# Performance work log

Measured on AMD Instinct MI355X. Metric: run time of the kernel, lower is better.

The kernel has to match this reference:

```python
import jax, jax.numpy as jnp
import numpy as np

B, C, H, W = 8, 512, 64, 64
M = C // 8  # query/key channels
EPS = 1e-6

def setup_inputs() -> dict:
    key = jax.random.key(0)
    ks = jax.random.split(key, 8)
    s_in = 0.02
    return {
        "x": jax.random.normal(ks[0], (B, C, H, W), dtype=jnp.float32),
        "Wq": jax.random.normal(ks[1], (M, C), dtype=jnp.float32) * s_in,
        "bq": jnp.zeros((M,), dtype=jnp.float32),
        "Wk": jax.random.normal(ks[2], (M, C), dtype=jnp.float32) * s_in,
        "bk": jnp.zeros((M,), dtype=jnp.float32),
        "Wv": jax.random.normal(ks[3], (C, C), dtype=jnp.float32) * s_in,
        "bv": jnp.zeros((C,), dtype=jnp.float32),
        "gamma": jax.random.uniform(ks[4], (1,), dtype=jnp.float32) * 0.5,
    }

def _l2_norm(t):
    # normalize over channel dim (axis=-2), per position; matches torch.norm(p=2, dim=-2)
    return t / jnp.linalg.norm(t, axis=-2, keepdims=True)

def reference(x, Wq, bq, Wk, bk, Wv, bv, gamma):
    b, c, h, w = x.shape
    n = h * w
    xf = x.reshape(b, c, n)                               # [b,c,n]
    # 1x1 convs as channel GEMMs
    Q = jnp.einsum('mc,bcn->bmn', Wq, xf) + bq[None, :, None]   # [b,m,n]
    K = jnp.einsum('mc,bcn->bmn', Wk, xf) + bk[None, :, None]   # [b,m,n]
    V = jnp.einsum('dc,bcn->bdn', Wv, xf) + bv[None, :, None]   # [b,c,n]
    Qn = _l2_norm(Q).transpose(0, 2, 1)                   # [b,n,m]
    Kn = _l2_norm(K)                                      # [b,m,n]
    # denominator: 1 / (N + Q . sum_n(K))
    tailor = 1.0 / (n + jnp.einsum('bnm,bm->bn', Qn, Kn.sum(axis=-1) + EPS))  # [b,n]
    value_sum = V.sum(axis=-1)                            # [b,c]
    matrix = jnp.einsum('bmn,bcn->bmc', Kn, V)            # [b,m,c] (O(N) contraction)
    matrix_sum = value_sum[:, :, None] + jnp.einsum('bnm,bmc->bcn', Qn, matrix)  # [b,c,n]
    weight_value = matrix_sum * tailor[:, None, :]        # [b,c,n]
    return x + gamma * weight_value.reshape(b, c, h, w)
```

## Files before the change

### kernel.cpp

```cpp
#include <hip/hip_runtime.h>
#include <hip/hip_bf16.h>

constexpr int B = 8;
constexpr int C = 512;
constexpr int M = 64;
constexpr int N = 4096;
constexpr float EPS = 1e-6f;
constexpr int NTS = 16;
constexpr int LDP = 72;
constexpr int LDPF = 68;

typedef __attribute__((ext_vector_type(8))) short short8v;
typedef __attribute__((ext_vector_type(4))) short short4v;
typedef __attribute__((ext_vector_type(4))) float f32x4;

__device__ __forceinline__ short f2b(float f) {
  union { __hip_bfloat16 h; short s; } u;
  u.h = __float2bfloat16(f);
  return u.s;
}
__device__ __forceinline__ float b2f(short s) {
  union { __hip_bfloat16 h; short s2; } u;
  u.s2 = s;
  return __bfloat162float(u.h);
}

__global__ __launch_bounds__(256) void prep_kernel(
    const float* __restrict__ Wq, const float* __restrict__ Wk,
    const float* __restrict__ Wv, short* __restrict__ Wq_bf,
    short* __restrict__ Wk_bf, short* __restrict__ Wv_bf,
    float* __restrict__ Ksum, float* __restrict__ xsum) {
  const int id = blockIdx.x * 256 + threadIdx.x;
  const int stride = gridDim.x * 256;
  for (int i = id; i < C * M / 4; i += stride) {
    const float4 a = reinterpret_cast<const float4*>(Wq)[i];
    const float4 b = reinterpret_cast<const float4*>(Wk)[i];
    short4v sa = {f2b(a.x), f2b(a.y), f2b(a.z), f2b(a.w)};
    short4v sb = {f2b(b.x), f2b(b.y), f2b(b.z), f2b(b.w)};
    reinterpret_cast<short4v*>(Wq_bf)[i] = sa;
    reinterpret_cast<short4v*>(Wk_bf)[i] = sb;
  }
  for (int i = id; i < C * C / 4; i += stride) {
    const float4 a = reinterpret_cast<const float4*>(Wv)[i];
    short4v sa = {f2b(a.x), f2b(a.y), f2b(a.z), f2b(a.w)};
    reinterpret_cast<short4v*>(Wv_bf)[i] = sa;
  }
  for (int i = id; i < B * M + B * C; i += stride) {
    if (i < B * M) Ksum[i] = 0.f;
    else xsum[i - B * M] = 0.f;
  }
}

__global__ __launch_bounds__(256) void qk_kernel(
    const float* __restrict__ x, const short* __restrict__ Wq_bf,
    const float* __restrict__ bq, const short* __restrict__ Wk_bf,
    const float* __restrict__ bk, short* __restrict__ QnT,
    short* __restrict__ KnB, float* __restrict__ Ksum) {
  __shared__ short aq[64 * LDP];
  __shared__ short ak[64 * LDP];
  __shared__ short bx[64 * LDP];
  __shared__ float colred[2][4][64];
  __shared__ float rsq[2][64];
  const int t = threadIdx.x;
  const int n0 = blockIdx.x * 64;
  const int b = blockIdx.y;
  const int w = t >> 6, l = t & 63, l15 = l & 15, kg = l >> 4;
  const int sr = t >> 2, sko = (t & 3) * 16;
  const int cr = t & 63, ng = t >> 6;
  f32x4 accQ[4], accK[4];
#pragma unroll
  for (int i = 0; i < 4; ++i) { accQ[i] = f32x4{0.f, 0.f, 0.f, 0.f}; accK[i] = f32x4{0.f, 0.f, 0.f, 0.f}; }

  short8v wq0, wq1, wk0, wk1;
  float4 xr[4];
  {
    wq0 = *reinterpret_cast<const short8v*>(&Wq_bf[sr * C + sko]);
    wq1 = *reinterpret_cast<const short8v*>(&Wq_bf[sr * C + sko + 8]);
    wk0 = *reinterpret_cast<const short8v*>(&Wk_bf[sr * C + sko]);
    wk1 = *reinterpret_cast<const short8v*>(&Wk_bf[sr * C + sko + 8]);
    const float* xg = x + ((size_t)b * C + cr) * N + n0 + ng * 16;
#pragma unroll
    for (int i = 0; i < 4; ++i) xr[i] = *reinterpret_cast<const float4*>(xg + 4 * i);
  }
  for (int c0 = 0; c0 < C; c0 += 64) {
    __syncthreads();
    *reinterpret_cast<short8v*>(&aq[sr * LDP + sko]) = wq0;
    *reinterpret_cast<short8v*>(&aq[sr * LDP + sko + 8]) = wq1;
    *reinterpret_cast<short8v*>(&ak[sr * LDP + sko]) = wk0;
    *reinterpret_cast<short8v*>(&ak[sr * LDP + sko + 8]) = wk1;
#pragma unroll
    for (int i = 0; i < 4; ++i) {
      bx[(ng * 16 + 4 * i + 0) * LDP + cr] = f2b(xr[i].x);
      bx[(ng * 16 + 4 * i + 1) * LDP + cr] = f2b(xr[i].y);
      bx[(ng * 16 + 4 * i + 2) * LDP + cr] = f2b(xr[i].z);
      bx[(ng * 16 + 4 * i + 3) * LDP + cr] = f2b(xr[i].w);
    }
    __syncthreads();
    if (c0 + 64 < C) {
      const int c1 = c0 + 64;
      wq0 = *reinterpret_cast<const short8v*>(&Wq_bf[sr * C + c1 + sko]);
      wq1 = *reinterpret_cast<const short8v*>(&Wq_bf[sr * C + c1 + sko + 8]);
      wk0 = *reinterpret_cast<const short8v*>(&Wk_bf[sr * C + c1 + sko]);
      wk1 = *reinterpret_cast<const short8v*>(&Wk_bf[sr * C + c1 + sko + 8]);
      const float* xg = x + ((size_t)b * C + c1 + cr) * N + n0 + ng * 16;
#pragma unroll
      for (int i = 0; i < 4; ++i) xr[i] = *reinterpret_cast<const float4*>(xg + 4 * i);
    }
#pragma unroll
    for (int ks = 0; ks < 2; ++ks) {
      const short8v afq = *reinterpret_cast<const short8v*>(&aq[(w * 16 + l15) * LDP + ks * 32 + kg * 8]);
      const short8v afk = *reinterpret_cast<const short8v*>(&ak[(w * 16 + l15) * LDP + ks * 32 + kg * 8]);
#pragma unroll
      for (int tc = 0; tc < 4; ++tc) {
        const short8v bf = *reinterpret_cast<const short8v*>(&bx[(tc * 16 + l15) * LDP + ks * 32 + kg * 8]);
        accQ[tc] = __builtin_amdgcn_mfma_f32_16x16x32_bf16(afq, bf, accQ[tc], 0, 0, 0);
        accK[tc] = __builtin_amdgcn_mfma_f32_16x16x32_bf16(afk, bf, accK[tc], 0, 0, 0);
      }
    }
  }
  {
    const float4 q4 = *reinterpret_cast<const float4*>(&bq[w * 16 + kg * 4]);
    const float4 k4 = *reinterpret_cast<const float4*>(&bk[w * 16 + kg * 4]);
    const float bqa[4] = {q4.x, q4.y, q4.z, q4.w};
    const float bka[4] = {k4.x, k4.y, k4.z, k4.w};
#pragma unroll
    for (int tc = 0; tc < 4; ++tc)
#pragma unroll
      for (int r = 0; r < 4; ++r) { accQ[tc][r] += bqa[r]; accK[tc][r] += bka[r]; }
  }
#pragma unroll
  for (int tc = 0; tc < 4; ++tc) {
    float vq = accQ[tc][0] * accQ[tc][0] + accQ[tc][1] * accQ[tc][1] +
               accQ[tc][2] * accQ[tc][2] + accQ[tc][3] * accQ[tc][3];
    float vk = accK[tc][0] * accK[tc][0] + accK[tc][1] * accK[tc][1] +
               accK[tc][2] * accK[tc][2] + accK[tc][3] * accK[tc][3];
    vq += __shfl_xor(vq, 16, 64); vq += __shfl_xor(vq, 32, 64);
    vk += __shfl_xor(vk, 16, 64); vk += __shfl_xor(vk, 32, 64);
    if (l < 16) { colred[0][w][tc * 16 + l] = vq; colred[1][w][tc * 16 + l] = vk; }
  }
  __syncthreads();
  if (t < 128) {
    const int which = t >> 6, n = t & 63;
    const float s = colred[which][0][n] + colred[which][1][n] +
                    colred[which][2][n] + colred[which][3][n];
    rsq[which][n] = 1.0f / sqrtf(s);
  }
  __syncthreads();
  float ksr[4] = {0.f, 0.f, 0.f, 0.f};
#pragma unroll
  for (int tc = 0; tc < 4; ++tc) {
    const float rq = rsq[0][tc * 16 + l15], rk = rsq[1][tc * 16 + l15];
#pragma unroll
    for (int r = 0; r < 4; ++r) { accQ[tc][r] *= rq; accK[tc][r] *= rk; ksr[r] += accK[tc][r]; }
  }
#pragma unroll
  for (int r = 0; r < 4; ++r) {
    float s = ksr[r];
    s += __shfl_xor(s, 1, 64); s += __shfl_xor(s, 2, 64);
    s += __shfl_xor(s, 4, 64); s += __shfl_xor(s, 8, 64);
    if (l15 == 0) atomicAdd(&Ksum[b * M + w * 16 + kg * 4 + r], s);
  }
#pragma unroll
  for (int tc = 0; tc < 4; ++tc) {
    short4v q4 = {f2b(accQ[tc][0]), f2b(accQ[tc][1]), f2b(accQ[tc][2]), f2b(accQ[tc][3])};
    *reinterpret_cast<short4v*>(&aq[(tc * 16 + l15) * LDP + w * 16 + kg * 4]) = q4;
#pragma unroll
    for (int r = 0; r < 4; ++r)
      ak[(w * 16 + kg * 4 + r) * LDP + tc * 16 + l15] = f2b(accK[tc][r]);
  }
  __syncthreads();
  {
    short* qg = QnT + ((size_t)b * N + n0 + sr) * M + sko;
    *reinterpret_cast<short8v*>(qg) = *reinterpret_cast<const short8v*>(&aq[sr * LDP + sko]);
    *reinterpret_cast<short8v*>(qg + 8) = *reinterpret_cast<const short8v*>(&aq[sr * LDP + sko + 8]);
    short* kg2 = KnB + ((size_t)b * M + sr) * N + n0 + sko;
    *reinterpret_cast<short8v*>(kg2) = *reinterpret_cast<const short8v*>(&ak[sr * LDP + sko]);
    *reinterpret_cast<short8v*>(kg2 + 8) = *reinterpret_cast<const short8v*>(&ak[sr * LDP + sko + 8]);
  }
}

__global__ __launch_bounds__(256) void s_kernel(
    const float* __restrict__ x, const short* __restrict__ KnB,
    short* __restrict__ Spart, float* __restrict__ xsum) {
  __shared__ short sm[2 * 64 * LDP];
  __shared__ float red[256];
  short* ka = sm;
  short* xb = sm + 64 * LDP;
  const int t = threadIdx.x;
  const int c0 = blockIdx.x * 64;
  const int nt = blockIdx.y;
  const int b = blockIdx.z;
  const int w = t >> 6, l = t & 63, l15 = l & 15, kg = l >> 4;
  const int sr = t >> 2, sko = (t & 3) * 16;
  f32x4 acc[4];
#pragma unroll
  for (int i = 0; i < 4; ++i) acc[i] = f32x4{0.f, 0.f, 0.f, 0.f};
  float xacc = 0.f;
  constexpr int ITERS = N / NTS / 64;
  const int nbase = nt * (N / NTS);
  short8v k0r, k1r;
  float4 xr[4];
  {
    const short* kp = &KnB[((size_t)b * M + sr) * N + nbase + sko];
    k0r = *reinterpret_cast<const short8v*>(kp);
    k1r = *reinterpret_cast<const short8v*>(kp + 8);
    const float* xg = x + ((size_t)b * C + c0 + sr) * N + nbase + sko;
#pragma unroll
    for (int i = 0; i < 4; ++i) xr[i] = *reinterpret_cast<const float4*>(xg + 4 * i);
  }
  for (int it = 0; it < ITERS; ++it) {
    __syncthreads();
    *reinterpret_cast<short8v*>(&ka[sr * LDP + sko]) = k0r;
    *reinterpret_cast<short8v*>(&ka[sr * LDP + sko + 8]) = k1r;
    short tmp[16];
#pragma unroll
    for (int i = 0; i < 4; ++i) {
      tmp[4 * i + 0] = f2b(xr[i].x); tmp[4 * i + 1] = f2b(xr[i].y);
      tmp[4 * i + 2] = f2b(xr[i].z); tmp[4 * i + 3] = f2b(xr[i].w);
      xacc += xr[i].x + xr[i].y + xr[i].z + xr[i].w;
    }
    *reinterpret_cast<short8v*>(&xb[sr * LDP + sko]) = *reinterpret_cast<const short8v*>(&tmp[0]);
    *reinterpret_cast<short8v*>(&xb[sr * LDP + sko + 8]) = *reinterpret_cast<const short8v*>(&tmp[8]);
    __syncthreads();
    if (it + 1 < ITERS) {
      const int nk = nbase + (it + 1) * 64;
      const short* kp = &KnB[((size_t)b * M + sr) * N + nk + sko];
      k0r = *reinterpret_cast<const short8v*>(kp);
      k1r = *reinterpret_cast<const short8v*>(kp + 8);
      const float* xg = x + ((size_t)b * C + c0 + sr) * N + nk + sko;
#pragma unroll
      for (int i = 0; i < 4; ++i) xr[i] = *reinterpret_cast<const float4*>(xg + 4 * i);
    }
#pragma unroll
    for (int ks = 0; ks < 2; ++ks) {
      const short8v af = *reinterpret_cast<const short8v*>(&ka[(w * 16 + l15) * LDP + ks * 32 + kg * 8]);
#pragma unroll
      for (int tc = 0; tc < 4; ++tc) {
        const short8v bf = *reinterpret_cast<const short8v*>(&xb[(tc * 16 + l15) * LDP + ks * 32 + kg * 8]);
        acc[tc] = __builtin_amdgcn_mfma_f32_16x16x32_bf16(af, bf, acc[tc], 0, 0, 0);
      }
    }
  }
  red[t] = xacc;
  __syncthreads();
  if (t < 64)
    atomicAdd(&xsum[b * C + c0 + t], red[4 * t] + red[4 * t + 1] + red[4 * t + 2] + red[4 * t + 3]);
#pragma unroll
  for (int tc = 0; tc < 4; ++tc)
#pragma unroll
    for (int r = 0; r < 4; ++r)
      sm[(w * 16 + kg * 4 + r) * LDP + tc * 16 + l15] = f2b(acc[tc][r]);
  __syncthreads();
  {
    short* gp = Spart + (((size_t)nt * B + b) * M + sr) * C + c0 + sko;
    *reinterpret_cast<short8v*>(gp) = *reinterpret_cast<const short8v*>(&sm[sr * LDP + sko]);
    *reinterpret_cast<short8v*>(gp + 8) = *reinterpret_cast<const short8v*>(&sm[sr * LDP + sko + 8]);
  }
}

__global__ __launch_bounds__(256) void matm_kernel(
    const short* __restrict__ Wv_bf, const float* __restrict__ bv,
    const short* __restrict__ Spart, const float* __restrict__ xsum,
    const float* __restrict__ Ksum, short* __restrict__ matMT,
    float* __restrict__ vsum) {
  __shared__ short wa[64 * LDP];
  __shared__ short sb[64 * LDP];
  __shared__ float xs[64];
  const int t = threadIdx.x;
  const int c0 = blockIdx.x * 64;
  const int b = blockIdx.y;
  const int w = t >> 6, l = t & 63, l15 = l & 15, kg = l >> 4;
  const int sr = t >> 2, sko = (t & 3) * 16;
  f32x4 acc[4];
#pragma unroll
  for (int i = 0; i < 4; ++i) acc[i] = f32x4{0.f, 0.f, 0.f, 0.f};
  float vacc = 0.f;
  for (int k0 = 0; k0 < C; k0 += 64) {
    __syncthreads();
    *reinterpret_cast<short8v*>(&wa[sr * LDP + sko]) =
        *reinterpret_cast<const short8v*>(&Wv_bf[(size_t)(c0 + sr) * C + k0 + sko]);
    *reinterpret_cast<short8v*>(&wa[sr * LDP + sko + 8]) =
        *reinterpret_cast<const short8v*>(&Wv_bf[(size_t)(c0 + sr) * C + k0 + sko + 8]);
    {
      float sacc[16];
#pragma unroll
      for (int j = 0; j < 16; ++j) sacc[j] = 0.f;
#pragma unroll 4
      for (int nt2 = 0; nt2 < NTS; ++nt2) {
        const short* sp = Spart + (((size_t)nt2 * B + b) * M + sr) * C + k0 + sko;
        const short8v p0 = *reinterpret_cast<const short8v*>(sp);
        const short8v p1 = *reinterpret_cast<const short8v*>(sp + 8);
#pragma unroll
        for (int j = 0; j < 8; ++j) { sacc[j] += b2f(p0[j]); sacc[8 + j] += b2f(p1[j]); }
      }
      short tmp[16];
#pragma unroll
      for (int j = 0; j < 16; ++j) tmp[j] = f2b(sacc[j]);
      *reinterpret_cast<short8v*>(&sb[sr * LDP + sko]) = *reinterpret_cast<const short8v*>(&tmp[0]);
      *reinterpret_cast<short8v*>(&sb[sr * LDP + sko + 8]) = *reinterpret_cast<const short8v*>(&tmp[8]);
    }
    if (t < 64) xs[t] = xsum[b * C + k0 + t];
    __syncthreads();
#pragma unroll
    for (int ks = 0; ks < 2; ++ks) {
      const short8v af = *reinterpret_cast<const short8v*>(&wa[(w * 16 + l15) * LDP + ks * 32 + kg * 8]);
#pragma unroll
      for (int tc = 0; tc < 4; ++tc) {
        const short8v bf = *reinterpret_cast<const short8v*>(&sb[(tc * 16 + l15) * LDP + ks * 32 + kg * 8]);
        acc[tc] = __builtin_amdgcn_mfma_f32_16x16x32_bf16(af, bf, acc[tc], 0, 0, 0);
      }
    }
    if (t < 64) {
      float v = 0.f;
#pragma unroll 8
      for (int kk = 0; kk < 64; ++kk) v = fmaf(b2f(wa[t * LDP + kk]), xs[kk], v);
      vacc += v;
    }
  }
  __syncthreads();
  {
    const float4 b4 = *reinterpret_cast<const float4*>(&bv[c0 + w * 16 + kg * 4]);
    const float bva[4] = {b4.x, b4.y, b4.z, b4.w};
#pragma unroll
    for (int tc = 0; tc < 4; ++tc) {
      const float ksm = Ksum[b * M + tc * 16 + l15];
#pragma unroll
      for (int r = 0; r < 4; ++r)
        wa[(w * 16 + kg * 4 + r) * LDP + tc * 16 + l15] = f2b(acc[tc][r] + bva[r] * ksm);
    }
  }
  __syncthreads();
  {
    short* gp = matMT + ((size_t)b * C + c0 + sr) * M + sko;
    *reinterpret_cast<short8v*>(gp) = *reinterpret_cast<const short8v*>(&wa[sr * LDP + sko]);
    *reinterpret_cast<short8v*>(gp + 8) = *reinterpret_cast<const short8v*>(&wa[sr * LDP + sko + 8]);
  }
  if (t < 64) vsum[b * C + c0 + t] = vacc + 4096.0f * bv[c0 + t];
}

__global__ __launch_bounds__(256) void final_kernel(
    const float* __restrict__ x, const short* __restrict__ QnT,
    const float* __restrict__ Ksum, const short* __restrict__ matMT,
    const float* __restrict__ vsum, const float* __restrict__ gamma,
    float* __restrict__ out) {
  __shared__ short qb[64 * LDP];
  __shared__ short ab[64 * LDP];
  __shared__ float bo[64 * LDPF];
  __shared__ float ke[64];
  __shared__ float tl[64];
  __shared__ float red2[256];
  const int t = threadIdx.x;
  const int n0 = blockIdx.x * 64;
  const int cy = blockIdx.y;
  const int b = blockIdx.z;
  const int w = t >> 6, l = t & 63, l15 = l & 15, kg = l >> 4;
  const int sr = t >> 2, sko = (t & 3) * 16;
  {
    const short* qg = &QnT[((size_t)b * N + n0 + sr) * M + sko];
    *reinterpret_cast<short8v*>(&qb[sr * LDP + sko]) = *reinterpret_cast<const short8v*>(qg);
    *reinterpret_cast<short8v*>(&qb[sr * LDP + sko + 8]) = *reinterpret_cast<const short8v*>(qg + 8);
  }
  if (t < 64) ke[t] = Ksum[b * M + t] + EPS;
  __syncthreads();
  {
    const int n = t & 63, mq = t >> 6;
    float d = 0.f;
#pragma unroll
    for (int j = 0; j < 16; ++j) d = fmaf(b2f(qb[n * LDP + mq * 16 + j]), ke[mq * 16 + j], d);
    red2[t] = d;
  }
  __syncthreads();
  if (t < 64)
    tl[t] = 1.0f / (4096.0f + red2[t] + red2[64 + t] + red2[128 + t] + red2[192 + t]);
  const float g = gamma[0];
  short8v ar0, ar1;
  {
    const short* mp = &matMT[((size_t)b * C + cy * 256 + sr) * M + sko];
    ar0 = *reinterpret_cast<const short8v*>(mp);
    ar1 = *reinterpret_cast<const short8v*>(mp + 8);
  }
  for (int cc = 0; cc < 4; ++cc) {
    const int c0 = cy * 256 + cc * 64;
    __syncthreads();
    *reinterpret_cast<short8v*>(&ab[sr * LDP + sko]) = ar0;
    *reinterpret_cast<short8v*>(&ab[sr * LDP + sko + 8]) = ar1;
    __syncthreads();
    if (cc < 3) {
      const short* mp = &matMT[((size_t)b * C + c0 + 64 + sr) * M + sko];
      ar0 = *reinterpret_cast<const short8v*>(mp);
      ar1 = *reinterpret_cast<const short8v*>(mp + 8);
    }
    float4 xr[4];
    {
      const float* xp = &x[((size_t)b * C + c0 + sr) * N + n0 + sko];
#pragma unroll
      for (int i = 0; i < 4; ++i) xr[i] = *reinterpret_cast<const float4*>(xp + 4 * i);
    }
    f32x4 acc[4];
#pragma unroll
    for (int i = 0; i < 4; ++i) acc[i] = f32x4{0.f, 0.f, 0.f, 0.f};
#pragma unroll
    for (int ks = 0; ks < 2; ++ks) {
      const short8v af = *reinterpret_cast<const short8v*>(&ab[(w * 16 + l15) * LDP + ks * 32 + kg * 8]);
#pragma unroll
      for (int tc = 0; tc < 4; ++tc) {
        const short8v bf = *reinterpret_cast<const short8v*>(&qb[(tc * 16 + l15) * LDP + ks * 32 + kg * 8]);
        acc[tc] = __builtin_amdgcn_mfma_f32_16x16x32_bf16(af, bf, acc[tc], 0, 0, 0);
      }
    }
#pragma unroll
    for (int tc = 0; tc < 4; ++tc)
#pragma unroll
      for (int r = 0; r < 4; ++r)
        bo[(w * 16 + kg * 4 + r) * LDPF + tc * 16 + l15] = acc[tc][r];
    __syncthreads();
    {
      const int c = c0 + sr;
      const float vs = vsum[b * C + c];
      const size_t off = ((size_t)b * C + c) * N + n0 + sko;
#pragma unroll
      for (int i = 0; i < 4; ++i) {
        const float4 dv = *reinterpret_cast<const float4*>(&bo[sr * LDPF + sko + 4 * i]);
        const float4 tv = *reinterpret_cast<const float4*>(&tl[sko + 4 * i]);
        float4 o;
        o.x = xr[i].x + g * tv.x * (vs + dv.x);
        o.y = xr[i].y + g * tv.y * (vs + dv.y);
        o.z = xr[i].z + g * tv.z * (vs + dv.z);
        o.w = xr[i].w + g * tv.w * (vs + dv.w);
        *reinterpret_cast<float4*>(&out[off + 4 * i]) = o;
      }
    }
  }
}

extern "C" void kernel_launch(void* const* d_in, const int* in_sizes, int n_in,
                              void* d_out, int out_size, void* d_ws, size_t ws_size,
                              hipStream_t stream) {
  (void)in_sizes; (void)n_in; (void)out_size; (void)ws_size;
  const float* x = (const float*)d_in[0];
  const float* Wq = (const float*)d_in[1];
  const float* bq = (const float*)d_in[2];
  const float* Wk = (const float*)d_in[3];
  const float* bk = (const float*)d_in[4];
  const float* Wv = (const float*)d_in[5];
  const float* bv = (const float*)d_in[6];
  const float* gamma = (const float*)d_in[7];
  float* out = (float*)d_out;

  char* wp = (char*)d_ws;
  short* Wq_bf = (short*)wp;  wp += (size_t)C * M * 2;
  short* Wk_bf = (short*)wp;  wp += (size_t)C * M * 2;
  short* Wv_bf = (short*)wp;  wp += (size_t)C * C * 2;
  short* KnB   = (short*)wp;  wp += (size_t)B * M * N * 2;
  short* QnT   = (short*)wp;  wp += (size_t)B * N * M * 2;
  short* matMT = (short*)wp;  wp += (size_t)B * C * M * 2;
  short* Spart = (short*)wp;  wp += (size_t)NTS * B * M * C * 2;
  float* Ksum  = (float*)wp;  wp += (size_t)B * M * 4;
  float* xsum  = (float*)wp;  wp += (size_t)B * C * 4;
  float* vsum  = (float*)wp;  wp += (size_t)B * C * 4;

  prep_kernel<<<256, 256, 0, stream>>>(Wq, Wk, Wv, Wq_bf, Wk_bf, Wv_bf, Ksum, xsum);
  qk_kernel<<<dim3(N / 64, B), 256, 0, stream>>>(x, Wq_bf, bq, Wk_bf, bk, QnT, KnB, Ksum);
  s_kernel<<<dim3(C / 64, NTS, B), 256, 0, stream>>>(x, KnB, Spart, xsum);
  matm_kernel<<<dim3(C / 64, B), 256, 0, stream>>>(Wv_bf, bv, Spart, xsum, Ksum, matMT, vsum);
  final_kernel<<<dim3(N / 64, 2, B), 256, 0, stream>>>(x, QnT, Ksum, matMT, vsum, gamma, out);
}
```

Measured before the change: 207.2 us.

## Precompute bf16 and transposed bf16 copies of x in a separate prep kernel

Adds a prepx kernel that reads x once and writes a bf16 copy, a transposed bf16 copy, and the per-channel sums. qk_kernel, s_kernel and final_kernel then load bf16 x instead of fp32 x, and the in-kernel conversion, the transpose and the register prefetch double-buffering are removed. The aim is to halve x read traffic in the three consumers and drop the conversion work there. In exchange it adds an extra kernel that writes two full bf16 copies of x, and loads are no longer overlapped with compute. The residual add in the final output now uses bf16-rounded x, which lowers accuracy.

```diff
diff --git a/kernel.cpp b/kernel.cpp
--- a/kernel.cpp
+++ b/kernel.cpp
@@ -51,8 +51,51 @@
   }
 }
 
+__global__ __launch_bounds__(256) void prepx_kernel(
+    const float* __restrict__ x, short* __restrict__ x_bf,
+    short* __restrict__ xT_bf, float* __restrict__ xsum) {
+  __shared__ short lt[64 * LDP];
+  __shared__ float red[256];
+  const int t = threadIdx.x;
+  const int nb = blockIdx.x * 64;
+  const int cb = blockIdx.y * 64;
+  const int b = blockIdx.z;
+  const int r = t >> 2, q = t & 3;
+  const float* xp = x + ((size_t)b * C + cb + r) * N + nb + q * 16;
+  float4 v[4];
+#pragma unroll
+  for (int i = 0; i < 4; ++i) v[i] = *reinterpret_cast<const float4*>(xp + 4 * i);
+  short tmp[16];
+  float s = 0.f;
+#pragma unroll
+  for (int i = 0; i < 4; ++i) {
+    tmp[4 * i + 0] = f2b(v[i].x); tmp[4 * i + 1] = f2b(v[i].y);
+    tmp[4 * i + 2] = f2b(v[i].z); tmp[4 * i + 3] = f2b(v[i].w);
+    s += v[i].x + v[i].y + v[i].z + v[i].w;
+  }
+  {
+    short* dst = x_bf + ((size_t)b * C + cb + r) * N + nb + q * 16;
+    *reinterpret_cast<short8v*>(dst) = *reinterpret_cast<const short8v*>(&tmp[0]);
+    *reinterpret_cast<short8v*>(dst + 8) = *reinterpret_cast<const short8v*>(&tmp[8]);
+  }
+#pragma unroll
+  for (int i = 0; i < 16; ++i) lt[(q * 16 + i) * LDP + r] = tmp[i];
+  red[t] = s;
+  __syncthreads();
+  if (t < 64) {
+    const float rs = red[4 * t] + red[4 * t + 1] + red[4 * t + 2] + red[4 * t + 3];
+    atomicAdd(&xsum[b * C + cb + t], rs);
+  }
+  {
+    const int n = t >> 2;
+    short* dst = xT_bf + ((size_t)b * N + nb + n) * C + cb + q * 16;
+    *reinterpret_cast<short8v*>(dst) = *reinterpret_cast<const short8v*>(&lt[n * LDP + q * 16]);
+    *reinterpret_cast<short8v*>(dst + 8) = *reinterpret_cast<const short8v*>(&lt[n * LDP + q * 16 + 8]);
+  }
+}
+
 __global__ __launch_bounds__(256) void qk_kernel(
-    const float* __restrict__ x, const short* __restrict__ Wq_bf,
+    const short* __restrict__ xT_bf, const short* __restrict__ Wq_bf,
     const float* __restrict__ bq, const short* __restrict__ Wk_bf,
     const float* __restrict__ bk, short* __restrict__ QnT,
     short* __restrict__ KnB, float* __restrict__ Ksum) {
@@ -66,46 +109,24 @@
   const int b = blockIdx.y;
   const int w = t >> 6, l = t & 63, l15 = l & 15, kg = l >> 4;
   const int sr = t >> 2, sko = (t & 3) * 16;
-  const int cr = t & 63, ng = t >> 6;
   f32x4 accQ[4], accK[4];
 #pragma unroll
   for (int i = 0; i < 4; ++i) { accQ[i] = f32x4{0.f, 0.f, 0.f, 0.f}; accK[i] = f32x4{0.f, 0.f, 0.f, 0.f}; }
 
-  short8v wq0, wq1, wk0, wk1;
-  float4 xr[4];
-  {
-    wq0 = *reinterpret_cast<const short8v*>(&Wq_bf[sr * C + sko]);
-    wq1 = *reinterpret_cast<const short8v*>(&Wq_bf[sr * C + sko + 8]);
-    wk0 = *reinterpret_cast<const short8v*>(&Wk_bf[sr * C + sko]);
-    wk1 = *reinterpret_cast<const short8v*>(&Wk_bf[sr * C + sko + 8]);
-    const float* xg = x + ((size_t)b * C + cr) * N + n0 + ng * 16;
-#pragma unroll
-    for (int i = 0; i < 4; ++i) xr[i] = *reinterpret_cast<const float4*>(xg + 4 * i);
-  }
   for (int c0 = 0; c0 < C; c0 += 64) {
     __syncthreads();
-    *reinterpret_cast<short8v*>(&aq[sr * LDP + sko]) = wq0;
-    *reinterpret_cast<short8v*>(&aq[sr * LDP + sko + 8]) = wq1;
-    *reinterpret_cast<short8v*>(&ak[sr * LDP + sko]) = wk0;
-    *reinterpret_cast<short8v*>(&ak[sr * LDP + sko + 8]) = wk1;
-#pragma unroll
-    for (int i = 0; i < 4; ++i) {
-      bx[(ng * 16 + 4 * i + 0) * LDP + cr] = f2b(xr[i].x);
-      bx[(ng * 16 + 4 * i + 1) * LDP + cr] = f2b(xr[i].y);
-      bx[(ng * 16 + 4 * i + 2) * LDP + cr] = f2b(xr[i].z);
-      bx[(ng * 16 + 4 * i + 3) * LDP + cr] = f2b(xr[i].w);
-    }
-    __syncthreads();
-    if (c0 + 64 < C) {
-      const int c1 = c0 + 64;
-      wq0 = *reinterpret_cast<const short8v*>(&Wq_bf[sr * C + c1 + sko]);
-      wq1 = *reinterpret_cast<const short8v*>(&Wq_bf[sr * C + c1 + sko + 8]);
-      wk0 = *reinterpret_cast<const short8v*>(&Wk_bf[sr * C + c1 + sko]);
-      wk1 = *reinterpret_cast<const short8v*>(&Wk_bf[sr * C + c1 + sko + 8]);
-      const float* xg = x + ((size_t)b * C + c1 + cr) * N + n0 + ng * 16;
-#pragma unroll
-      for (int i = 0; i < 4; ++i) xr[i] = *reinterpret_cast<const float4*>(xg + 4 * i);
-    }
+    *reinterpret_cast<short8v*>(&aq[sr * LDP + sko]) =
+        *reinterpret_cast<const short8v*>(&Wq_bf[sr * C + c0 + sko]);
+    *reinterpret_cast<short8v*>(&aq[sr * LDP + sko + 8]) =
+        *reinterpret_cast<const short8v*>(&Wq_bf[sr * C + c0 + sko + 8]);
+    *reinterpret_cast<short8v*>(&ak[sr * LDP + sko]) =
+        *reinterpret_cast<const short8v*>(&Wk_bf[sr * C + c0 + sko]);
+    *reinterpret_cast<short8v*>(&ak[sr * LDP + sko + 8]) =
+        *reinterpret_cast<const short8v*>(&Wk_bf[sr * C + c0 + sko + 8]);
+    const short* xg = &xT_bf[((size_t)b * N + n0 + sr) * C + c0 + sko];
+    *reinterpret_cast<short8v*>(&bx[sr * LDP + sko]) = *reinterpret_cast<const short8v*>(xg);
+    *reinterpret_cast<short8v*>(&bx[sr * LDP + sko + 8]) = *reinterpret_cast<const short8v*>(xg + 8);
+    __syncthreads();
 #pragma unroll
     for (int ks = 0; ks < 2; ++ks) {
       const short8v afq = *reinterpret_cast<const short8v*>(&aq[(w * 16 + l15) * LDP + ks * 32 + kg * 8]);
@@ -180,10 +201,9 @@
 }
 
 __global__ __launch_bounds__(256) void s_kernel(
-    const float* __restrict__ x, const short* __restrict__ KnB,
-    short* __restrict__ Spart, float* __restrict__ xsum) {
+    const short* __restrict__ x_bf, const short* __restrict__ KnB,
+    short* __restrict__ Spart) {
   __shared__ short sm[2 * 64 * LDP];
-  __shared__ float red[256];
   short* ka = sm;
   short* xb = sm + 64 * LDP;
   const int t = threadIdx.x;
@@ -195,42 +215,20 @@
   f32x4 acc[4];
 #pragma unroll
   for (int i = 0; i < 4; ++i) acc[i] = f32x4{0.f, 0.f, 0.f, 0.f};
-  float xacc = 0.f;
   constexpr int ITERS = N / NTS / 64;
   const int nbase = nt * (N / NTS);
-  short8v k0r, k1r;
-  float4 xr[4];
-  {
-    const short* kp = &KnB[((size_t)b * M + sr) * N + nbase + sko];
-    k0r = *reinterpret_cast<const short8v*>(kp);
-    k1r = *reinterpret_cast<const short8v*>(kp + 8);
-    const float* xg = x + ((size_t)b * C + c0 + sr) * N + nbase + sko;
-#pragma unroll
-    for (int i = 0; i < 4; ++i) xr[i] = *reinterpret_cast<const float4*>(xg + 4 * i);
-  }
   for (int it = 0; it < ITERS; ++it) {
-    __syncthreads();
-    *reinterpret_cast<short8v*>(&ka[sr * LDP + sko]) = k0r;
-    *reinterpret_cast<short8v*>(&ka[sr * LDP + sko + 8]) = k1r;
-    short tmp[16];
-#pragma unroll
-    for (int i = 0; i < 4; ++i) {
-      tmp[4 * i + 0] = f2b(xr[i].x); tmp[4 * i + 1] = f2b(xr[i].y);
-      tmp[4 * i + 2] = f2b(xr[i].z); tmp[4 * i + 3] = f2b(xr[i].w);
-      xacc += xr[i].x + xr[i].y + xr[i].z + xr[i].w;
-    }
-    *reinterpret_cast<short8v*>(&xb[sr * LDP + sko]) = *reinterpret_cast<const short8v*>(&tmp[0]);
-    *reinterpret_cast<short8v*>(&xb[sr * LDP + sko + 8]) = *reinterpret_cast<const short8v*>(&tmp[8]);
-    __syncthreads();
-    if (it + 1 < ITERS) {
-      const int nk = nbase + (it + 1) * 64;
+    const int nk = nbase + it * 64;
+    __syncthreads();
+    {
       const short* kp = &KnB[((size_t)b * M + sr) * N + nk + sko];
-      k0r = *reinterpret_cast<const short8v*>(kp);
-      k1r = *reinterpret_cast<const short8v*>(kp + 8);
-      const float* xg = x + ((size_t)b * C + c0 + sr) * N + nk + sko;
-#pragma unroll
-      for (int i = 0; i < 4; ++i) xr[i] = *reinterpret_cast<const float4*>(xg + 4 * i);
-    }
+      *reinterpret_cast<short8v*>(&ka[sr * LDP + sko]) = *reinterpret_cast<const short8v*>(kp);
+      *reinterpret_cast<short8v*>(&ka[sr * LDP + sko + 8]) = *reinterpret_cast<const short8v*>(kp + 8);
+      const short* xp = &x_bf[((size_t)b * C + c0 + sr) * N + nk + sko];
+      *reinterpret_cast<short8v*>(&xb[sr * LDP + sko]) = *reinterpret_cast<const short8v*>(xp);
+      *reinterpret_cast<short8v*>(&xb[sr * LDP + sko + 8]) = *reinterpret_cast<const short8v*>(xp + 8);
+    }
+    __syncthreads();
 #pragma unroll
     for (int ks = 0; ks < 2; ++ks) {
       const short8v af = *reinterpret_cast<const short8v*>(&ka[(w * 16 + l15) * LDP + ks * 32 + kg * 8]);
@@ -241,10 +239,7 @@
       }
     }
   }
-  red[t] = xacc;
-  __syncthreads();
-  if (t < 64)
-    atomicAdd(&xsum[b * C + c0 + t], red[4 * t] + red[4 * t + 1] + red[4 * t + 2] + red[4 * t + 3]);
+  __syncthreads();
 #pragma unroll
   for (int tc = 0; tc < 4; ++tc)
 #pragma unroll
@@ -339,7 +334,7 @@
 }
 
 __global__ __launch_bounds__(256) void final_kernel(
-    const float* __restrict__ x, const short* __restrict__ QnT,
+    const short* __restrict__ x_bf, const short* __restrict__ QnT,
     const float* __restrict__ Ksum, const short* __restrict__ matMT,
     const float* __restrict__ vsum, const float* __restrict__ gamma,
     float* __restrict__ out) {
@@ -373,28 +368,20 @@
   if (t < 64)
     tl[t] = 1.0f / (4096.0f + red2[t] + red2[64 + t] + red2[128 + t] + red2[192 + t]);
   const float g = gamma[0];
-  short8v ar0, ar1;
-  {
-    const short* mp = &matMT[((size_t)b * C + cy * 256 + sr) * M + sko];
-    ar0 = *reinterpret_cast<const short8v*>(mp);
-    ar1 = *reinterpret_cast<const short8v*>(mp + 8);
-  }
   for (int cc = 0; cc < 4; ++cc) {
     const int c0 = cy * 256 + cc * 64;
     __syncthreads();
-    *reinterpret_cast<short8v*>(&ab[sr * LDP + sko]) = ar0;
-    *reinterpret_cast<short8v*>(&ab[sr * LDP + sko + 8]) = ar1;
-    __syncthreads();
-    if (cc < 3) {
-      const short* mp = &matMT[((size_t)b * C + c0 + 64 + sr) * M + sko];
-      ar0 = *reinterpret_cast<const short8v*>(mp);
-      ar1 = *reinterpret_cast<const short8v*>(mp + 8);
-    }
-    float4 xr[4];
     {
-      const float* xp = &x[((size_t)b * C + c0 + sr) * N + n0 + sko];
-#pragma unroll
-      for (int i = 0; i < 4; ++i) xr[i] = *reinterpret_cast<const float4*>(xp + 4 * i);
+      const short* mp = &matMT[((size_t)b * C + c0 + sr) * M + sko];
+      *reinterpret_cast<short8v*>(&ab[sr * LDP + sko]) = *reinterpret_cast<const short8v*>(mp);
+      *reinterpret_cast<short8v*>(&ab[sr * LDP + sko + 8]) = *reinterpret_cast<const short8v*>(mp + 8);
+    }
+    __syncthreads();
+    short8v xr0, xr1;
+    {
+      const short* xp = &x_bf[((size_t)b * C + c0 + sr) * N + n0 + sko];
+      xr0 = *reinterpret_cast<const short8v*>(xp);
+      xr1 = *reinterpret_cast<const short8v*>(xp + 8);
     }
     f32x4 acc[4];
 #pragma unroll
@@ -423,10 +410,10 @@
         const float4 dv = *reinterpret_cast<const float4*>(&bo[sr * LDPF + sko + 4 * i]);
         const float4 tv = *reinterpret_cast<const float4*>(&tl[sko + 4 * i]);
         float4 o;
-        o.x = xr[i].x + g * tv.x * (vs + dv.x);
-        o.y = xr[i].y + g * tv.y * (vs + dv.y);
-        o.z = xr[i].z + g * tv.z * (vs + dv.z);
-        o.w = xr[i].w + g * tv.w * (vs + dv.w);
+        o.x = b2f(i * 4 + 0 < 8 ? xr0[i * 4 + 0] : xr1[i * 4 - 8]) + g * tv.x * (vs + dv.x);
+        o.y = b2f(i * 4 + 1 < 8 ? xr0[(i * 4 + 1) & 7] : xr1[(i * 4 + 1) & 7]) + g * tv.y * (vs + dv.y);
+        o.z = b2f(i * 4 + 2 < 8 ? xr0[(i * 4 + 2) & 7] : xr1[(i * 4 + 2) & 7]) + g * tv.z * (vs + dv.z);
+        o.w = b2f(i * 4 + 3 < 8 ? xr0[(i * 4 + 3) & 7] : xr1[(i * 4 + 3) & 7]) + g * tv.w * (vs + dv.w);
         *reinterpret_cast<float4*>(&out[off + 4 * i]) = o;
       }
     }
@@ -451,6 +438,8 @@
   short* Wq_bf = (short*)wp;  wp += (size_t)C * M * 2;
   short* Wk_bf = (short*)wp;  wp += (size_t)C * M * 2;
   short* Wv_bf = (short*)wp;  wp += (size_t)C * C * 2;
+  short* x_bf  = (short*)wp;  wp += (size_t)B * C * N * 2;
+  short* xT_bf = (short*)wp;  wp += (size_t)B * N * C * 2;
   short* KnB   = (short*)wp;  wp += (size_t)B * M * N * 2;
   short* QnT   = (short*)wp;  wp += (size_t)B * N * M * 2;
   short* matMT = (short*)wp;  wp += (size_t)B * C * M * 2;
@@ -460,8 +449,9 @@
   float* vsum  = (float*)wp;  wp += (size_t)B * C * 4;
 
   prep_kernel<<<256, 256, 0, stream>>>(Wq, Wk, Wv, Wq_bf, Wk_bf, Wv_bf, Ksum, xsum);
-  qk_kernel<<<dim3(N / 64, B), 256, 0, stream>>>(x, Wq_bf, bq, Wk_bf, bk, QnT, KnB, Ksum);
-  s_kernel<<<dim3(C / 64, NTS, B), 256, 0, stream>>>(x, KnB, Spart, xsum);
+  prepx_kernel<<<dim3(N / 64, C / 64, B), 256, 0, stream>>>(x, x_bf, xT_bf, xsum);
+  qk_kernel<<<dim3(N / 64, B), 256, 0, stream>>>(xT_bf, Wq_bf, bq, Wk_bf, bk, QnT, KnB, Ksum);
+  s_kernel<<<dim3(C / 64, NTS, B), 256, 0, stream>>>(x_bf, KnB, Spart);
   matm_kernel<<<dim3(C / 64, B), 256, 0, stream>>>(Wv_bf, bv, Spart, xsum, Ksum, matMT, vsum);
-  final_kernel<<<dim3(N / 64, 2, B), 256, 0, stream>>>(x, QnT, Ksum, matMT, vsum, gamma, out);
-}
+  final_kernel<<<dim3(N / 64, 2, B), 256, 0, stream>>>(x_bf, QnT, Ksum, matMT, vsum, gamma, out);
+}
```

Result: slower. 220.2 us (+6.3%).
